# Kernel optimization log

Hardware: AMD Instinct MI355X
Metric: run time of the kernel (lower is better)

The kernel has to match this reference:

```python
import jax, jax.numpy as jnp
import numpy as np

NUM_CLASSES = 80
SCORE_THRESH = 0.5
NMS_THRESH = 0.5
TOP_K = 200  # max candidates kept per (image, class) before greedy NMS


def setup_inputs() -> dict:
    key = jax.random.key(0)
    k1, k2, k3 = jax.random.split(key, 3)
    B, A, HW, C = 8, 3, 5776, NUM_CLASSES  # 608-input YOLOv4 P3 level: 76*76
    # well-formed boxes in [0,1]: x1y1 + positive wh
    xy = jax.random.uniform(k1, (B, A, HW, 2)) * 0.8
    wh = jax.random.uniform(k2, (B, A, HW, 2)) * 0.2 + 0.01
    boxes = jnp.concatenate([xy, xy + wh], axis=-1)
    scores = jax.random.uniform(k3, (B, A, HW, C))
    return {"boxes": boxes, "scores": scores}


def _pairwise_iou(b):
    # b: [K, 4] (x1, y1, x2, y2) -> IoU matrix [K, K] (union mode)
    x1, y1, x2, y2 = b[:, 0], b[:, 1], b[:, 2], b[:, 3]
    area = (x2 - x1) * (y2 - y1)
    xx1 = jnp.maximum(x1[:, None], x1[None, :])
    yy1 = jnp.maximum(y1[:, None], y1[None, :])
    xx2 = jnp.minimum(x2[:, None], x2[None, :])
    yy2 = jnp.minimum(y2[:, None], y2[None, :])
    inter = jnp.maximum(0.0, xx2 - xx1) * jnp.maximum(0.0, yy2 - yy1)
    return inter / (area[:, None] + area[None, :] - inter)


def _nms_one(boxes, scores):
    # boxes: [N, 4], scores: [N] -> top-K candidates with greedy-NMS keep mask
    s = jnp.where(scores > SCORE_THRESH, scores, -jnp.inf)  # score threshold filter
    top_s, idx = jax.lax.top_k(s, TOP_K)                    # descending, like argsort()[::-1]
    b = boxes[idx]                                          # [K, 4]
    valid = jnp.isfinite(top_s)
    iou = _pairwise_iou(b)                                  # [K, K]

    def body(keep, i):
        # if box i survives, suppress all lower-scored boxes with IoU > thresh
        sup = keep[i] & (iou[i] > NMS_THRESH) & (jnp.arange(TOP_K) > i)
        return keep & ~sup, None

    keep, _ = jax.lax.scan(body, valid, jnp.arange(TOP_K))
    return b, top_s, keep


def reference(boxes, scores):
    B, A, HW, _ = boxes.shape
    C = scores.shape[-1]
    b = boxes.reshape(B, A * HW, 4)
    s = scores.reshape(B, A * HW, C)
    per_img = jax.vmap(lambda bb, ss: jax.vmap(_nms_one, in_axes=(None, 1))(bb, ss))
    boxes_k, scores_k, keep = per_img(b, s)  # [B,C,K,4], [B,C,K], [B,C,K]
    cls = jnp.broadcast_to(jnp.arange(C, dtype=boxes.dtype)[None, :, None], keep.shape)
    out_box = jnp.where(keep[..., None], boxes_k, 0.0)
    out_score = jnp.where(keep, scores_k, 0.0)
    out_cls = jnp.where(keep, cls, 0.0)
    # padded detections [B, C, K, 6] = (x1, y1, x2, y2, score, class_id)
    return jnp.concatenate([out_box, out_score[..., None], out_cls[..., None]], axis=-1)
```

## Files before the change

### kernel.cpp

```cpp
#include <hip/hip_runtime.h>
#include <stdint.h>

#define B_IMG  8
#define NANCH  17328
#define NCLS   80
#define TOPK   200
#define NTHR   256
#define NTHRB  512
#define CHUNK  64
#define NCHK   ((NANCH + CHUNK - 1) / CHUNK)
#define NCHKP  272
#define SLOT   12
#define NPOS   (NCHK * SLOT)
#define NBC    (B_IMG * NCLS)
#define THRESH_HI 0.98f

__device__ __forceinline__ void hist_add(float s, unsigned int* hist) {
  if (s > 0.5f) {
    unsigned int bin = (__float_as_uint(s) - 0x3F000000u) >> 15;
    if (bin > 255u) bin = 255u;
    atomicAdd(&hist[bin], 1u);
  }
}

__global__ __launch_bounds__(NTHR) void scatter_k(
    const float* __restrict__ scores,
    unsigned char* __restrict__ cnt2,
    unsigned long long* __restrict__ cand) {
  const int nb = blockIdx.x;
  const int b  = blockIdx.y;
  const int tid = threadIdx.x;
  const int wv = tid >> 6, lane = tid & 63;
  const int n0 = nb * CHUNK;

  __shared__ float tile[CHUNK][81];

  const int nrow = (NANCH - n0 < CHUNK) ? (NANCH - n0) : CHUNK;
  const int nf4 = nrow * (NCLS / 4);
  const float4* src4 = (const float4*)(scores + (size_t)(b * NANCH + n0) * NCLS);
  for (int f = tid; f < nf4; f += NTHR) {
    float4 v = src4[f];
    int n = f / 20, c4 = (f - n * 20) * 4;
    tile[n][c4] = v.x; tile[n][c4 + 1] = v.y;
    tile[n][c4 + 2] = v.z; tile[n][c4 + 3] = v.w;
  }
  __syncthreads();

  const bool rv = (lane < nrow);
  const unsigned long long lt = (1ull << lane) - 1ull;
  const int cbase = wv * 20;
#pragma unroll 4
  for (int cc = 0; cc < 20; ++cc) {
    const int c = cbase + cc;
    const int bc = b * NCLS + c;
    float s = rv ? tile[lane][c] : 0.f;
    const bool cd = (s > THRESH_HI);
    unsigned long long bal = __ballot(cd);
    if (cd) {
      unsigned int r = (unsigned int)__popcll(bal & lt);
      if (r < SLOT)
        cand[((size_t)bc * NCHK + nb) * SLOT + r] =
            ((unsigned long long)__float_as_uint(s) << 32) |
            (unsigned long long)(0xFFFFFFFFu - (unsigned int)(n0 + lane));
    }
    if (lane == 0)
      cnt2[(size_t)bc * NCHKP + nb] = (unsigned char)__popcll(bal);
  }
}

__global__ __launch_bounds__(NTHRB) void backend_k(
    const float* __restrict__ scores, const float* __restrict__ boxes,
    const unsigned char* __restrict__ cnt2, const unsigned long long* __restrict__ cand,
    float* __restrict__ out) {
  const int bc = blockIdx.x;
  const int b = bc / NCLS;
  const int c = bc - b * NCLS;
  const int tid = threadIdx.x;
  const int wv = tid >> 6, lane = tid & 63;
  const unsigned long long lt = (1ull << lane) - 1ull;

  __shared__ unsigned long long selk[512];
  __shared__ unsigned int hist[256];
  __shared__ float sx1[256], sy1[256], sx2[256], sy2[256], sar[256], ssc[256];
  __shared__ int skeep[256];
  __shared__ __align__(16) unsigned long long sup[TOPK][4];
  __shared__ __align__(16) float eout[TOPK * 6];
  __shared__ unsigned int sh_cutbits;
  __shared__ int sh_sel, sh_bad;

  if (tid == 0) { sh_sel = 0; sh_bad = 0; }
  __syncthreads();

  const unsigned long long* cb0 = cand + (size_t)bc * NCHK * SLOT;
  const unsigned char* ct0 = cnt2 + (size_t)bc * NCHKP;
  for (int p = tid; p < NPOS; p += NTHRB) {
    const int ch = p / SLOT;
    const int sl = p - ch * SLOT;
    unsigned int ci = (unsigned int)ct0[ch];
    if (sl == 0 && ci > SLOT) sh_bad = 1;
    unsigned long long k = 0ull;
    bool pred = (sl < (int)ci);
    if (pred) k = cb0[p];
    unsigned long long bal = __ballot(pred);
    if (bal) {
      int base0 = 0;
      if (lane == 0) base0 = atomicAdd(&sh_sel, (int)__popcll(bal));
      base0 = __shfl(base0, 0, 64);
      if (pred) {
        int pos = base0 + (int)__popcll(bal & lt);
        if (pos < 512) selk[pos] = k;
      }
    }
  }
  __syncthreads();

  int Msel = sh_sel;
  const bool fb = (sh_bad != 0) || (Msel < TOPK) || (Msel > 512);

  if (fb) {
    if (tid < 256) hist[tid] = 0u;
    if (tid == 0) sh_sel = 0;
    __syncthreads();
    const float* src = scores + (size_t)b * NANCH * NCLS + c;
    for (int i = tid; i < NANCH; i += NTHRB) hist_add(src[(size_t)i * NCLS], hist);
    __syncthreads();
    if (tid == 0) {
      unsigned int acc = 0;
      int cut = 0;
      for (int bin = 255; bin >= 0; --bin) {
        acc += hist[bin];
        if (acc >= TOPK) { cut = bin; break; }
      }
      sh_cutbits = 0x3F000000u + ((unsigned int)cut << 15);
    }
    __syncthreads();
    const unsigned int cutbits = sh_cutbits;
    for (int i = tid; i < NANCH; i += NTHRB) {
      float s = src[(size_t)i * NCLS];
      if (s > 0.5f && __float_as_uint(s) >= cutbits) {
        int slot = atomicAdd(&sh_sel, 1);
        if (slot < 512)
          selk[slot] = ((unsigned long long)__float_as_uint(s) << 32) |
                       (unsigned long long)(0xFFFFFFFFu - (unsigned int)i);
      }
    }
    __syncthreads();
    Msel = sh_sel; if (Msel > 512) Msel = 512;
  }

  const int S = (Msel <= 256) ? 256 : 512;
  for (int j = Msel + tid; j < S; j += NTHRB) selk[j] = 0ull;

  for (int size = 2; size <= S; size <<= 1) {
    for (int st = size >> 1; st > 0; st >>= 1) {
      __syncthreads();
      for (int t = tid; t < (S >> 1); t += NTHRB) {
        int lo = 2 * t - (t & (st - 1));
        int hi = lo + st;
        bool desc = ((lo & size) == 0);
        unsigned long long a = selk[lo], bb = selk[hi];
        if ((a < bb) == desc) { selk[lo] = bb; selk[hi] = a; }
      }
    }
  }
  __syncthreads();

  if (tid < 256) {
    unsigned long long key = selk[tid];
    int valid = (tid < TOPK) && (key != 0ull);
    unsigned int idx = 0xFFFFFFFFu - (unsigned int)(key & 0xFFFFFFFFull);
    float4 bx = make_float4(0.f, 0.f, 0.f, 0.f);
    if (valid) bx = ((const float4*)boxes)[(size_t)b * NANCH + idx];
    sx1[tid] = bx.x; sy1[tid] = bx.y; sx2[tid] = bx.z; sy2[tid] = bx.w;
    sar[tid] = __fmul_rn(bx.z - bx.x, bx.w - bx.y);
    ssc[tid] = valid ? __uint_as_float((unsigned int)(key >> 32)) : 0.f;
    skeep[tid] = valid;
  }
  __syncthreads();

  {
    float jx1[4], jy1[4], jx2[4], jy2[4], ja[4];
#pragma unroll
    for (int r = 0; r < 4; ++r) {
      int j = (r << 6) | lane;
      jx1[r] = sx1[j]; jy1[r] = sy1[j]; jx2[r] = sx2[j]; jy2[r] = sy2[j];
      ja[r] = sar[j];
    }
    float nx1 = sx1[wv], ny1 = sy1[wv], nx2 = sx2[wv], ny2 = sy2[wv], na = sar[wv];
    for (int k = 0; k < 25; ++k) {
      const int i = (k << 3) + wv;
      const float xi1 = nx1, yi1 = ny1, xi2 = nx2, yi2 = ny2, ai = na;
      const int inx = i + 8;
      if (inx < TOPK) {
        nx1 = sx1[inx]; ny1 = sy1[inx]; nx2 = sx2[inx]; ny2 = sy2[inx];
        na = sar[inx];
      }
      const int d = i >> 6;
      const int il = i & 63;
      unsigned long long dmask = (il == 63) ? 0ull : ((~0ull) << (il + 1));
      if (d == 3) dmask &= 0xFFull;
      unsigned long long w[4];
#pragma unroll
      for (int r = 0; r < 4; ++r) {
        unsigned long long word = 0ull;
        if ((r << 6) + 63 > i) {
          const unsigned long long wmask =
              (r > d) ? ((r == 3) ? 0xFFull : ~0ull) : dmask;
          float xx1 = fmaxf(xi1, jx1[r]);
          float yy1 = fmaxf(yi1, jy1[r]);
          float xx2 = fminf(xi2, jx2[r]);
          float yy2 = fminf(yi2, jy2[r]);
          float iw = fmaxf(0.f, __fsub_rn(xx2, xx1));
          float ih = fmaxf(0.f, __fsub_rn(yy2, yy1));
          float inter = __fmul_rn(iw, ih);
          float denom = __fsub_rn(__fadd_rn(ai, ja[r]), inter);
          float q = __fmul_rn(inter, __builtin_amdgcn_rcpf(denom));
          word = __ballot(q > 0.5f);
          unsigned long long gb = __ballot(fabsf(q - 0.5f) < 1e-5f) & wmask;
          if (gb)
            word = __ballot(__fdiv_rn(inter, denom) > 0.5f);
          word &= wmask;
        }
        w[r] = word;
      }
      if (lane == 0) {
        ulonglong2* dst = (ulonglong2*)&sup[i][0];
        ulonglong2 t0; t0.x = w[0]; t0.y = w[1];
        ulonglong2 t1; t1.x = w[2]; t1.y = w[3];
        dst[0] = t0; dst[1] = t1;
      }
    }
  }
  __syncthreads();

  if (tid < 64) {
    unsigned long long k0 = __ballot(skeep[tid] != 0);
    unsigned long long k1 = __ballot(skeep[64 + tid] != 0);
    unsigned long long k2 = __ballot(skeep[128 + tid] != 0);
    unsigned long long k3 = __ballot(skeep[192 + tid] != 0);
#define NMS_SCAN_WORD(KW, BASE, CNT)                                     \
    _Pragma("unroll 8")                                                  \
    for (int li = 0; li < (CNT); ++li) {                                 \
      const ulonglong2* s2p =                                            \
          reinterpret_cast<const ulonglong2*>(&sup[(BASE) + li][0]);     \
      ulonglong2 sa = s2p[0];                                            \
      ulonglong2 sb = s2p[1];                                            \
      unsigned long long m = 0ull - ((KW >> li) & 1ull);                 \
      k0 &= ~(sa.x & m); k1 &= ~(sa.y & m);                              \
      k2 &= ~(sb.x & m); k3 &= ~(sb.y & m);                              \
    }
    NMS_SCAN_WORD(k0, 0, 64)
    NMS_SCAN_WORD(k1, 64, 64)
    NMS_SCAN_WORD(k2, 128, 64)
    NMS_SCAN_WORD(k3, 192, 8)
#undef NMS_SCAN_WORD
    skeep[tid]        = (int)((k0 >> tid) & 1ull);
    skeep[64 + tid]   = (int)((k1 >> tid) & 1ull);
    skeep[128 + tid]  = (int)((k2 >> tid) & 1ull);
    skeep[192 + tid]  = (int)((k3 >> tid) & 1ull);
  }
  __syncthreads();

  if (tid < TOPK) {
    int kp = skeep[tid];
    eout[tid * 6 + 0] = kp ? sx1[tid] : 0.f;
    eout[tid * 6 + 1] = kp ? sy1[tid] : 0.f;
    eout[tid * 6 + 2] = kp ? sx2[tid] : 0.f;
    eout[tid * 6 + 3] = kp ? sy2[tid] : 0.f;
    eout[tid * 6 + 4] = kp ? ssc[tid] : 0.f;
    eout[tid * 6 + 5] = kp ? (float)c : 0.f;
  }
  __syncthreads();

  float4* out4 = (float4*)(out + (size_t)bc * (TOPK * 6));
  const float4* e4 = (const float4*)eout;
  for (int f = tid; f < (TOPK * 6) / 4; f += NTHRB) out4[f] = e4[f];
}

__global__ __launch_bounds__(NTHR) void select_nms_k(
    const float* __restrict__ boxes, const float* __restrict__ scores,
    float* __restrict__ out) {
  const int blk = blockIdx.x;
  const int b = blk / NCLS;
  const int c = blk - b * NCLS;
  const int tid = threadIdx.x;

  __shared__ unsigned int hist[256];
  __shared__ unsigned long long keys[1024];
  __shared__ float sx1[TOPK], sy1[TOPK], sx2[TOPK], sy2[TOPK], sar[TOPK], ssc[TOPK];
  __shared__ int skeep[TOPK];
  __shared__ unsigned int sh_cutbits;
  __shared__ int sh_m;

  const float* src = scores + (size_t)b * NANCH * NCLS + c;

  for (int j = tid; j < 256; j += NTHR) hist[j] = 0;
  if (tid == 0) sh_m = 0;
  __syncthreads();

  for (int i = tid; i < NANCH; i += NTHR) hist_add(src[(size_t)i * NCLS], hist);
  __syncthreads();

  if (tid == 0) {
    unsigned int acc = 0;
    int cut = 0;
    for (int bin = 255; bin >= 0; --bin) {
      acc += hist[bin];
      if (acc >= TOPK) { cut = bin; break; }
    }
    sh_cutbits = 0x3F000000u + ((unsigned int)cut << 15);
  }
  __syncthreads();
  const unsigned int cutbits = sh_cutbits;

  for (int i = tid; i < NANCH; i += NTHR) {
    float s = src[(size_t)i * NCLS];
    if (s > 0.5f && __float_as_uint(s) >= cutbits) {
      int slot = atomicAdd(&sh_m, 1);
      if (slot < 1024)
        keys[slot] = ((unsigned long long)__float_as_uint(s) << 32) |
                     (unsigned long long)(0xFFFFFFFFu - (unsigned int)i);
    }
  }
  __syncthreads();
  int M = sh_m; if (M > 1024) M = 1024;
  for (int j = M + tid; j < 1024; j += NTHR) keys[j] = 0ull;

  for (int size = 2; size <= 1024; size <<= 1) {
    for (int st = size >> 1; st > 0; st >>= 1) {
      __syncthreads();
      for (int t = tid; t < 512; t += NTHR) {
        int lo = 2 * t - (t & (st - 1));
        int hi = lo + st;
        bool desc = ((lo & size) == 0);
        unsigned long long a = keys[lo], bb = keys[hi];
        if ((a < bb) == desc) { keys[lo] = bb; keys[hi] = a; }
      }
    }
  }
  __syncthreads();

  if (tid < TOPK) {
    unsigned long long key = keys[tid];
    int valid = (key != 0ull);
    float sc = __uint_as_float((unsigned int)(key >> 32));
    unsigned int idx = 0xFFFFFFFFu - (unsigned int)(key & 0xFFFFFFFFull);
    float4 bx = make_float4(0.f, 0.f, 0.f, 0.f);
    if (valid) bx = ((const float4*)boxes)[(size_t)b * NANCH + idx];
    sx1[tid] = bx.x; sy1[tid] = bx.y; sx2[tid] = bx.z; sy2[tid] = bx.w;
    sar[tid] = __fmul_rn(bx.z - bx.x, bx.w - bx.y);
    ssc[tid] = valid ? sc : 0.f;
    skeep[tid] = valid;
  }
  __syncthreads();

  if (tid < 64) {
    const int lane = tid;
    float x1v[4], y1v[4], x2v[4], y2v[4], av[4];
    int km = 0;
#pragma unroll
    for (int r = 0; r < 4; ++r) {
      int j = lane + (r << 6);
      if (j < TOPK) {
        x1v[r] = sx1[j]; y1v[r] = sy1[j]; x2v[r] = sx2[j]; y2v[r] = sy2[j];
        av[r] = sar[j];
        if (skeep[j]) km |= (1 << r);
      } else {
        x1v[r] = 0.f; y1v[r] = 0.f; x2v[r] = 0.f; y2v[r] = 0.f; av[r] = 0.f;
      }
    }
#pragma unroll
    for (int ri = 0; ri < 4; ++ri) {
      const int imax = (ri == 3) ? (TOPK - 192) : 64;
      for (int li = 0; li < imax; ++li) {
        const int i = (ri << 6) + li;
        int kmi = __shfl(km, li, 64);
        if (!((kmi >> ri) & 1)) continue;
        float xi1 = __shfl(x1v[ri], li, 64);
        float yi1 = __shfl(y1v[ri], li, 64);
        float xi2 = __shfl(x2v[ri], li, 64);
        float yi2 = __shfl(y2v[ri], li, 64);
        float ai  = __shfl(av[ri],  li, 64);
#pragma unroll
        for (int r = 0; r < 4; ++r) {
          int j = lane + (r << 6);
          if (j > i && j < TOPK && ((km >> r) & 1)) {
            float xx1 = fmaxf(xi1, x1v[r]);
            float yy1 = fmaxf(yi1, y1v[r]);
            float xx2 = fminf(xi2, x2v[r]);
            float yy2 = fminf(yi2, y2v[r]);
            float iw = fmaxf(0.f, __fsub_rn(xx2, xx1));
            float ih = fmaxf(0.f, __fsub_rn(yy2, yy1));
            float inter = __fmul_rn(iw, ih);
            float denom = __fsub_rn(__fadd_rn(ai, av[r]), inter);
            float iou = __fdiv_rn(inter, denom);
            if (iou > 0.5f) km &= ~(1 << r);
          }
        }
      }
    }
#pragma unroll
    for (int r = 0; r < 4; ++r) {
      int j = lane + (r << 6);
      if (j < TOPK) skeep[j] = (km >> r) & 1;
    }
  }
  __syncthreads();

  const size_t base = ((size_t)b * NCLS + c) * (TOPK * 6);
  for (int f = tid; f < TOPK * 6; f += NTHR) {
    int k = f / 6, comp = f - k * 6;
    float v = 0.f;
    if (skeep[k]) {
      switch (comp) {
        case 0: v = sx1[k]; break;
        case 1: v = sy1[k]; break;
        case 2: v = sx2[k]; break;
        case 3: v = sy2[k]; break;
        case 4: v = ssc[k]; break;
        default: v = (float)c; break;
      }
    }
    out[base + f] = v;
  }
}

extern "C" void kernel_launch(void* const* d_in, const int* in_sizes, int n_in,
                              void* d_out, int out_size, void* d_ws, size_t ws_size,
                              hipStream_t stream) {
  (void)in_sizes; (void)n_in; (void)out_size;
  const float* boxes  = (const float*)d_in[0];
  const float* scores = (const float*)d_in[1];
  float* out = (float*)d_out;

  const size_t need_c2 = (size_t)NBC * NCHKP;
  const size_t need_cd = (size_t)NBC * NCHK * SLOT * sizeof(uint64_t);
  const size_t need = need_c2 + need_cd;

  if (ws_size >= need) {
    char* w = (char*)d_ws;
    unsigned char* cnt2      = (unsigned char*)w;       w += need_c2;
    unsigned long long* cand = (unsigned long long*)w;

    scatter_k<<<dim3(NCHK, B_IMG), NTHR, 0, stream>>>(scores, cnt2, cand);
    backend_k<<<NBC, NTHRB, 0, stream>>>(scores, boxes, cnt2, cand, out);
  } else {
    select_nms_k<<<NBC, NTHR, 0, stream>>>(boxes, scores, out);
  }
}
```

Measured before the change: 72.84 us.

## Compute NMS IoU suppression matrix per-thread with shared atomicOr instead of ballots

```diff
diff --git a/kernel.cpp b/kernel.cpp
--- a/kernel.cpp
+++ b/kernel.cpp
@@ -76,12 +76,13 @@
   const int b = bc / NCLS;
   const int c = bc - b * NCLS;
   const int tid = threadIdx.x;
-  const int wv = tid >> 6, lane = tid & 63;
+  const int lane = tid & 63;
   const unsigned long long lt = (1ull << lane) - 1ull;
 
   __shared__ unsigned long long selk[512];
   __shared__ unsigned int hist[256];
-  __shared__ float sx1[256], sy1[256], sx2[256], sy2[256], sar[256], ssc[256];
+  __shared__ __align__(16) float4 sbox[256];
+  __shared__ float sar[256], ssc[256];
   __shared__ int skeep[256];
   __shared__ __align__(16) unsigned long long sup[TOPK][4];
   __shared__ __align__(16) float eout[TOPK * 6];
@@ -171,63 +172,43 @@
     unsigned int idx = 0xFFFFFFFFu - (unsigned int)(key & 0xFFFFFFFFull);
     float4 bx = make_float4(0.f, 0.f, 0.f, 0.f);
     if (valid) bx = ((const float4*)boxes)[(size_t)b * NANCH + idx];
-    sx1[tid] = bx.x; sy1[tid] = bx.y; sx2[tid] = bx.z; sy2[tid] = bx.w;
+    sbox[tid] = bx;
     sar[tid] = __fmul_rn(bx.z - bx.x, bx.w - bx.y);
     ssc[tid] = valid ? __uint_as_float((unsigned int)(key >> 32)) : 0.f;
     skeep[tid] = valid;
+  } else {
+    unsigned long long* sw = (unsigned long long*)&sup[0][0];
+    for (int f = tid - 256; f < TOPK * 4; f += 256) sw[f] = 0ull;
   }
   __syncthreads();
 
   {
-    float jx1[4], jy1[4], jx2[4], jy2[4], ja[4];
-#pragma unroll
-    for (int r = 0; r < 4; ++r) {
-      int j = (r << 6) | lane;
-      jx1[r] = sx1[j]; jy1[r] = sy1[j]; jx2[r] = sx2[j]; jy2[r] = sy2[j];
-      ja[r] = sar[j];
-    }
-    float nx1 = sx1[wv], ny1 = sy1[wv], nx2 = sx2[wv], ny2 = sy2[wv], na = sar[wv];
-    for (int k = 0; k < 25; ++k) {
-      const int i = (k << 3) + wv;
-      const float xi1 = nx1, yi1 = ny1, xi2 = nx2, yi2 = ny2, ai = na;
-      const int inx = i + 8;
-      if (inx < TOPK) {
-        nx1 = sx1[inx]; ny1 = sy1[inx]; nx2 = sx2[inx]; ny2 = sy2[inx];
-        na = sar[inx];
-      }
-      const int d = i >> 6;
-      const int il = i & 63;
-      unsigned long long dmask = (il == 63) ? 0ull : ((~0ull) << (il + 1));
-      if (d == 3) dmask &= 0xFFull;
-      unsigned long long w[4];
-#pragma unroll
-      for (int r = 0; r < 4; ++r) {
-        unsigned long long word = 0ull;
-        if ((r << 6) + 63 > i) {
-          const unsigned long long wmask =
-              (r > d) ? ((r == 3) ? 0xFFull : ~0ull) : dmask;
-          float xx1 = fmaxf(xi1, jx1[r]);
-          float yy1 = fmaxf(yi1, jy1[r]);
-          float xx2 = fminf(xi2, jx2[r]);
-          float yy2 = fminf(yi2, jy2[r]);
-          float iw = fmaxf(0.f, __fsub_rn(xx2, xx1));
-          float ih = fmaxf(0.f, __fsub_rn(yy2, yy1));
-          float inter = __fmul_rn(iw, ih);
-          float denom = __fsub_rn(__fadd_rn(ai, ja[r]), inter);
-          float q = __fmul_rn(inter, __builtin_amdgcn_rcpf(denom));
-          word = __ballot(q > 0.5f);
-          unsigned long long gb = __ballot(fabsf(q - 0.5f) < 1e-5f) & wmask;
-          if (gb)
-            word = __ballot(__fdiv_rn(inter, denom) > 0.5f);
-          word &= wmask;
-        }
-        w[r] = word;
-      }
-      if (lane == 0) {
-        ulonglong2* dst = (ulonglong2*)&sup[i][0];
-        ulonglong2 t0; t0.x = w[0]; t0.y = w[1];
-        ulonglong2 t1; t1.x = w[2]; t1.y = w[3];
-        dst[0] = t0; dst[1] = t1;
+    unsigned long long* sw = (unsigned long long*)&sup[0][0];
+    for (int t2 = tid; t2 < 1600; t2 += NTHRB) {
+      const int i = t2 >> 3;
+      const int j0 = (t2 & 7) * 25;
+      if (j0 + 24 <= i) continue;
+      const float4 bi = sbox[i];
+      const float ai = sar[i];
+#pragma unroll 5
+      for (int q = 0; q < 25; ++q) {
+        const int j = j0 + q;
+        if (j <= i) continue;
+        const float4 bj = sbox[j];
+        float xx1 = fmaxf(bi.x, bj.x);
+        float yy1 = fmaxf(bi.y, bj.y);
+        float xx2 = fminf(bi.z, bj.z);
+        float yy2 = fminf(bi.w, bj.w);
+        float iw = fmaxf(0.f, __fsub_rn(xx2, xx1));
+        float ih = fmaxf(0.f, __fsub_rn(yy2, yy1));
+        float inter = __fmul_rn(iw, ih);
+        float denom = __fsub_rn(__fadd_rn(ai, sar[j]), inter);
+        float qq = __fmul_rn(inter, __builtin_amdgcn_rcpf(denom));
+        bool s = qq > 0.5f;
+        if (fabsf(qq - 0.5f) < 1e-5f)
+          s = __fdiv_rn(inter, denom) > 0.5f;
+        if (s)
+          atomicOr(&sw[i * 4 + (j >> 6)], 1ull << (j & 63));
       }
     }
   }
@@ -263,10 +244,11 @@
 
   if (tid < TOPK) {
     int kp = skeep[tid];
-    eout[tid * 6 + 0] = kp ? sx1[tid] : 0.f;
-    eout[tid * 6 + 1] = kp ? sy1[tid] : 0.f;
-    eout[tid * 6 + 2] = kp ? sx2[tid] : 0.f;
-    eout[tid * 6 + 3] = kp ? sy2[tid] : 0.f;
+    float4 bx = sbox[tid];
+    eout[tid * 6 + 0] = kp ? bx.x : 0.f;
+    eout[tid * 6 + 1] = kp ? bx.y : 0.f;
+    eout[tid * 6 + 2] = kp ? bx.z : 0.f;
+    eout[tid * 6 + 3] = kp ? bx.w : 0.f;
     eout[tid * 6 + 4] = kp ? ssc[tid] : 0.f;
     eout[tid * 6 + 5] = kp ? (float)c : 0.f;
   }
```

Result: slower. 75.87 us (+4.2%).
